# Kernel optimization log

Hardware: AMD Instinct MI355X
Metric: run time of the kernel (lower is better)

Reference implementation:

```python
import jax, jax.numpy as jnp
import numpy as np

B, C, H, W = 4, 256, 64, 64
CH = C // 2  # inner channels of the non-local block


def _conv1x1(x, w, b):
    # 1x1 conv == channel-mixing einsum; x: [B,C,H,W], w: [O,C], b: [O]
    return jnp.einsum('oc,bchw->bohw', w, x) + b[None, :, None, None]


def setup_inputs() -> dict:
    key = jax.random.key(0)
    ks = jax.random.split(key, 9)
    s = 0.02  # small init so exp(scores) stays in fp32 range (no max-subtraction in this block)
    return {
        'x':  jax.random.normal(ks[0], (B, C, H, W), dtype=jnp.float32),
        'w1': s * jax.random.normal(ks[1], (CH, C), dtype=jnp.float32),
        'b1': jnp.zeros((CH,), jnp.float32),
        'w2': s * jax.random.normal(ks[2], (CH, C), dtype=jnp.float32),
        'b2': jnp.zeros((CH,), jnp.float32),
        'w3': s * jax.random.normal(ks[3], (CH, C), dtype=jnp.float32),
        'b3': jnp.zeros((CH,), jnp.float32),
        'w4': s * jax.random.normal(ks[4], (C, CH), dtype=jnp.float32),
        'b4': jnp.zeros((C,), jnp.float32),
    }


def reference(x, w1, b1, w2, b2, w3, b3, w4, b4):
    b, c, h, w = x.shape
    n = h * w
    theta = _conv1x1(x, w1, b1).reshape(b, -1, n)  # [B, C/2, N]
    phi   = _conv1x1(x, w2, b2).reshape(b, -1, n)  # [B, C/2, N]
    g     = _conv1x1(x, w3, b3).reshape(b, -1, n)  # [B, C/2, N]
    # full non-local affinity: [B, N, N]
    scores = jnp.einsum('bci,bcj->bij', theta, phi)
    attn = jnp.exp(scores)  # faithful: no max-subtraction in the original
    attn = attn / jnp.sum(attn, axis=1, keepdims=True)  # normalize over dim=1 as written
    y = jnp.einsum('bij,bcj->bci', attn, g)  # [B, C/2, N]
    y = y.reshape(b, -1, h, w)               # [B, C/2, H, W]
    out = _conv1x1(y, w4, b4) + x            # project back to C, residual
    return out
```

## Files before the change

### kernel.cpp

```cpp
#include <hip/hip_runtime.h>

#define DEVI __device__ __forceinline__

typedef __attribute__((ext_vector_type(8))) short bf16x8;
typedef __attribute__((ext_vector_type(4))) short bf16x4;
typedef __attribute__((ext_vector_type(4))) float f32x4;

#define MFMA16 __builtin_amdgcn_mfma_f32_16x16x32_bf16

#define ASM_WAIT_VM_LGKM(n) asm volatile("s_waitcnt vmcnt(" #n ") lgkmcnt(0)" ::: "memory")
#define ASM_WAIT_LGKM() asm volatile("s_waitcnt lgkmcnt(0)" ::: "memory")
#define ASM_BARRIER() do { __builtin_amdgcn_s_barrier(); asm volatile("" ::: "memory"); } while (0)

DEVI short f2bs(float f) {
  union { float f; unsigned u; } v; v.f = f;
  unsigned r = v.u + 0x7fffu + ((v.u >> 16) & 1u);
  return (short)(r >> 16);
}
DEVI float bs2f(short s) {
  union { unsigned u; float f; } v; v.u = ((unsigned)(unsigned short)s) << 16;
  return v.f;
}

DEVI void gload_lds16(const short* g, short* lds) {
  __builtin_amdgcn_global_load_lds(
      (const __attribute__((address_space(1))) unsigned int*)g,
      (__attribute__((address_space(3))) unsigned int*)lds, 16, 0, 0);
}


DEVI void stage_chunk(short* lds, const short* g, int ldg, int tid) {
#pragma unroll
  for (int it = 0; it < 2; ++it) {
    int slot = it * 256 + tid;
    int row  = slot >> 2;
    int ko   = ((slot ^ (slot >> 3)) & 3) << 3;
    gload_lds16(g + (size_t)row * ldg + ko, lds + slot * 8);
  }
}

DEVI void stage_chunk64(short* lds, const short* g, int ldg, int tid) {
  int row = tid >> 2;
  int ko  = ((tid ^ (tid >> 3)) & 3) << 3;
  gload_lds16(g + (size_t)row * ldg + ko, lds + tid * 8);
}

DEVI bf16x8 lds8(const short* p) { return *(const bf16x8*)p; }

DEVI void zero_acc(f32x4 (&a)[4][4]) {
  f32x4 z = {0.f, 0.f, 0.f, 0.f};
#pragma unroll
  for (int i = 0; i < 4; ++i)
#pragma unroll
    for (int j = 0; j < 4; ++j) a[i][j] = z;
}

__global__ __launch_bounds__(256) void k_transpose_cast(const float* __restrict__ x,
                                                        short* __restrict__ xt) {
  __shared__ float t[64][65];
  int b = blockIdx.z;
  int c0 = blockIdx.y * 64;
  int p0 = blockIdx.x * 64;
  int tid = threadIdx.x;
  const float* xb = x + (size_t)b * 256 * 4096;
#pragma unroll
  for (int i = 0; i < 16; ++i) {
    int idx = i * 256 + tid;
    int c = idx >> 6, p = idx & 63;
    t[p][c] = xb[(size_t)(c0 + c) * 4096 + p0 + p];
  }
  __syncthreads();
  short* xtb = xt + ((size_t)b * 4096 + p0) * 256 + c0;
#pragma unroll
  for (int i = 0; i < 16; ++i) {
    int idx = i * 256 + tid;
    int p = idx >> 6, c = idx & 63;
    xtb[(size_t)p * 256 + c] = f2bs(t[p][c]);
  }
}

__global__ __launch_bounds__(256) void k_cast_w(const float* __restrict__ w1,
                                                const float* __restrict__ w2,
                                                const float* __restrict__ w3,
                                                short* __restrict__ w123) {
  int i = blockIdx.x * 256 + threadIdx.x;
  if (i < 384 * 256) {
    int r = i >> 8;
    const float* w = (r < 128) ? w1 : (r < 256 ? w2 : w3);
    w123[i] = f2bs(w[(size_t)(r & 127) * 256 + (i & 255)]);
  }
}

__global__ __launch_bounds__(256) void k_proj(const short* __restrict__ xt,
                                              const short* __restrict__ w123,
                                              const float* __restrict__ b1,
                                              const float* __restrict__ b2,
                                              const float* __restrict__ b3,
                                              short* __restrict__ theta,
                                              short* __restrict__ phi,
                                              short* __restrict__ gbuf) {
  __shared__ short aL[2][4096];
  __shared__ short bL[2][4096];
  __shared__ short oL[128 * 136];
  int tid = threadIdx.x;
  int m0 = blockIdx.x * 128;
  int nb = blockIdx.y;
  int b  = blockIdx.z;
  int lane = tid & 63, wid = tid >> 6;
  int col = lane & 15, quad = lane >> 4;
  int sl = (col >> 1) & 3;
  int qs = (quad ^ sl) << 3;
  int wm = (wid >> 1) * 64, wn = (wid & 1) * 64;
  const short* A = xt + ((size_t)b * 4096 + m0) * 256;
  const short* B = w123 + (size_t)nb * 128 * 256;
  f32x4 acc[4][4];
  zero_acc(acc);
  stage_chunk(&aL[0][0], A, 256, tid);
  stage_chunk(&bL[0][0], B, 256, tid);
  for (int ks = 0; ks < 8; ++ks) {
    int cur = ks & 1;
    ASM_WAIT_VM_LGKM(0);
    ASM_BARRIER();
    if (ks < 7) {
      stage_chunk(&aL[cur ^ 1][0], A + (ks + 1) * 32, 256, tid);
      stage_chunk(&bL[cur ^ 1][0], B + (ks + 1) * 32, 256, tid);
    }
    bf16x8 af[4], bf_[4];
#pragma unroll
    for (int mi = 0; mi < 4; ++mi) af[mi] = lds8(&aL[cur][(wm + mi * 16 + col) * 32 + qs]);
#pragma unroll
    for (int ni = 0; ni < 4; ++ni) bf_[ni] = lds8(&bL[cur][(wn + ni * 16 + col) * 32 + qs]);
    __builtin_amdgcn_s_setprio(1);
#pragma unroll
    for (int mi = 0; mi < 4; ++mi)
#pragma unroll
      for (int ni = 0; ni < 4; ++ni)
        acc[mi][ni] = MFMA16(af[mi], bf_[ni], acc[mi][ni], 0, 0, 0);
    __builtin_amdgcn_s_setprio(0);
  }
  const float* bias = (nb == 0) ? b1 : (nb == 1 ? b2 : b3);
#pragma unroll
  for (int mi = 0; mi < 4; ++mi)
#pragma unroll
    for (int ni = 0; ni < 4; ++ni) {
      float bv = bias[wn + ni * 16 + col];
#pragma unroll
      for (int r = 0; r < 4; ++r)
        oL[(wm + mi * 16 + quad * 4 + r) * 136 + wn + ni * 16 + col] = f2bs(acc[mi][ni][r] + bv);
    }
  __syncthreads();
  short* O = ((nb == 0) ? theta : (nb == 1) ? phi : gbuf) + ((size_t)b * 4096 + m0) * 128;
#pragma unroll
  for (int it = 0; it < 8; ++it) {
    int slot = it * 256 + tid;
    int r = slot >> 4, cp = (slot & 15) * 8;
    *(bf16x8*)(O + (size_t)r * 128 + cp) = lds8(&oL[r * 136 + cp]);
  }
}

__global__ __launch_bounds__(256, 2) void k_denom(const short* __restrict__ theta,
                                                  const short* __restrict__ phi,
                                                  float* __restrict__ dpart) {
  __shared__ short phB[2][16384];
  __shared__ float part[1024];
  int tid = threadIdx.x;
  int ib = blockIdx.x, jc = blockIdx.y, b = blockIdx.z;
  int lane = tid & 63, wid = tid >> 6;
  int col = lane & 15, quad = lane >> 4;
  int sl = (col >> 1) & 3;
  int qs = (quad ^ sl) << 3;
  int wm = (wid >> 1) * 64, wn = (wid & 1) * 64;
  const short* T = theta + ((size_t)b * 4096 + ib * 128) * 128;
  const short* P = phi + ((size_t)b * 4096 + (size_t)jc * 1024) * 128;
  float* dbase = dpart + ((size_t)(b * 32 + ib)) * 4096 + jc * 1024;
  short* Lb = &phB[0][0];
#pragma unroll
  for (int ks = 0; ks < 4; ++ks) stage_chunk(Lb + ks * 8192, T + ks * 32, 128, tid);
  __syncthreads();
  bf16x8 ath[4][4];
#pragma unroll
  for (int ks = 0; ks < 4; ++ks)
#pragma unroll
    for (int mi = 0; mi < 4; ++mi)
      ath[ks][mi] = lds8(&Lb[ks * 8192 + (wm + mi * 16 + col) * 32 + qs]);
  __syncthreads();
#pragma unroll
  for (int ks = 0; ks < 4; ++ks) stage_chunk(&phB[0][0] + ks * 4096, P + ks * 32, 128, tid);
  float dval = 0.f;
  for (int jt = 0; jt < 8; ++jt) {
    int cur = jt & 1;
    ASM_WAIT_VM_LGKM(0);
    ASM_BARRIER();
    if (jt > 0 && tid < 128) dbase[(jt - 1) * 128 + tid] = dval;
    if (jt < 7) {
      const short* Pn = P + (size_t)(jt + 1) * 128 * 128;
#pragma unroll
      for (int ks = 0; ks < 4; ++ks) stage_chunk(&phB[cur ^ 1][0] + ks * 4096, Pn + ks * 32, 128, tid);
    }
    f32x4 sacc[4][4];
    zero_acc(sacc);
#pragma unroll
    for (int ks = 0; ks < 4; ++ks) {
      bf16x8 bp[4];
#pragma unroll
      for (int ni = 0; ni < 4; ++ni) bp[ni] = lds8(&phB[cur][ks * 4096 + (wn + ni * 16 + col) * 32 + qs]);
      __builtin_amdgcn_s_setprio(1);
#pragma unroll
      for (int mi = 0; mi < 4; ++mi)
#pragma unroll
        for (int ni = 0; ni < 4; ++ni)
          sacc[mi][ni] = MFMA16(ath[ks][mi], bp[ni], sacc[mi][ni], 0, 0, 0);
      __builtin_amdgcn_s_setprio(0);
    }
#pragma unroll
    for (int ni = 0; ni < 4; ++ni) {
      float s = 0.f;
#pragma unroll
      for (int mi = 0; mi < 4; ++mi)
#pragma unroll
        for (int r = 0; r < 4; ++r) s += __expf(sacc[mi][ni][r]);
      part[((wid >> 1) * 4 + quad) * 128 + wn + ni * 16 + col] = s;
    }
    ASM_WAIT_LGKM();
    ASM_BARRIER();
    if (tid < 128) {
      float d = 0.f;
#pragma unroll
      for (int q = 0; q < 8; ++q) d += part[q * 128 + tid];
      dval = d;
    }
  }
  if (tid < 128) dbase[7 * 128 + tid] = dval;
}

__global__ __launch_bounds__(256) void k_fold(const short* __restrict__ gbuf,
                                              const float* __restrict__ dpart,
                                              short* __restrict__ gprime) {
  __shared__ float dinv[128];
  __shared__ short t[128 * 136];
  int tid = threadIdx.x;
  int jb = blockIdx.x, b = blockIdx.y;
  int j0 = jb * 128;
  if (tid < 128) {
    float d = 0.f;
    for (int ib = 0; ib < 32; ++ib) d += dpart[((size_t)(b * 32 + ib)) * 4096 + j0 + tid];
    dinv[tid] = 1.0f / d;
  }
  __syncthreads();
  const short* G = gbuf + ((size_t)b * 4096 + j0) * 128;
#pragma unroll
  for (int it = 0; it < 8; ++it) {
    int slot = it * 256 + tid;
    int j = slot >> 4, c8 = (slot & 15) * 8;
    bf16x8 gv = *(const bf16x8*)(G + (size_t)j * 128 + c8);
    float di = dinv[j];
#pragma unroll
    for (int e = 0; e < 8; ++e) t[(c8 + e) * 136 + j] = f2bs(bs2f(gv[e]) * di);
  }
  __syncthreads();
  short* GP = gprime + (size_t)b * 128 * 4096 + j0;
#pragma unroll
  for (int it = 0; it < 8; ++it) {
    int slot = it * 256 + tid;
    int c = slot >> 4, j8 = (slot & 15) * 8;
    *(bf16x8*)(GP + (size_t)c * 4096 + j8) = *(const bf16x8*)&t[c * 136 + j8];
  }
}

__global__ __launch_bounds__(256, 2) void k_attn_pv(const short* __restrict__ theta,
                                                    const short* __restrict__ phi,
                                                    const short* __restrict__ gprime,
                                                    short* __restrict__ ypart) {
  __shared__ short L[40960];
  int tid = threadIdx.x;
  int ib = blockIdx.x, jc = blockIdx.y, b = blockIdx.z;
  int lane = tid & 63, wid = tid >> 6;
  int col = lane & 15, quad = lane >> 4;
  int sl = (col >> 1) & 3;
  int qs = (quad ^ sl) << 3;
  int wm = (wid >> 1) * 64;
  int cj = wid & 1;
  int wnS = cj * 32;
  int wnV = cj * 64;
  const short* T = theta + ((size_t)b * 4096 + ib * 128) * 128;
  const short* PH = phi + ((size_t)b * 4096 + (size_t)jc * 1024) * 128;
  const short* GP = gprime + (size_t)b * 128 * 4096 + jc * 1024;
  short* pP = L + 32768;
#pragma unroll
  for (int ks = 0; ks < 4; ++ks) stage_chunk(L + ks * 8192, T + ks * 32, 128, tid);
  __syncthreads();
  bf16x8 ath[4][4];
#pragma unroll
  for (int ks = 0; ks < 4; ++ks)
#pragma unroll
    for (int mi = 0; mi < 4; ++mi)
      ath[ks][mi] = lds8(&L[ks * 8192 + (wm + mi * 16 + col) * 32 + qs]);
  __syncthreads();
#pragma unroll
  for (int ks = 0; ks < 4; ++ks) stage_chunk64(L + ks * 2048, PH + ks * 32, 128, tid);
#pragma unroll
  for (int jh = 0; jh < 2; ++jh) stage_chunk(L + 16384 + jh * 4096, GP + jh * 32, 4096, tid);
  f32x4 accy[4][4];
  zero_acc(accy);
  int qh = quad >> 1, ql = (quad & 1) << 2;
  for (int jt = 0; jt < 16; ++jt) {
    int cur = jt & 1;
    short* phc = L + cur * 8192;
    short* phn = L + (cur ^ 1) * 8192;
    short* gpc = L + 16384 + cur * 8192;
    short* gpn = L + 16384 + (cur ^ 1) * 8192;
    ASM_WAIT_VM_LGKM(4);
    ASM_BARRIER();
    if (jt < 15) {
      const short* PHn = PH + (size_t)(jt + 1) * 64 * 128;
#pragma unroll
      for (int ks = 0; ks < 4; ++ks) stage_chunk64(phn + ks * 2048, PHn + ks * 32, 128, tid);
    }
    f32x4 st[2][4];
#pragma unroll
    for (int mj = 0; mj < 2; ++mj)
#pragma unroll
      for (int ni = 0; ni < 4; ++ni) st[mj][ni] = (f32x4){0.f, 0.f, 0.f, 0.f};
#pragma unroll
    for (int ks = 0; ks < 4; ++ks) {
      bf16x8 bp[2];
#pragma unroll
      for (int mj = 0; mj < 2; ++mj)
        bp[mj] = lds8(&phc[ks * 2048 + (wnS + mj * 16 + col) * 32 + qs]);
      __builtin_amdgcn_s_setprio(1);
#pragma unroll
      for (int mj = 0; mj < 2; ++mj)
#pragma unroll
        for (int ni = 0; ni < 4; ++ni)
          st[mj][ni] = MFMA16(bp[mj], ath[ks][ni], st[mj][ni], 0, 0, 0);
      __builtin_amdgcn_s_setprio(0);
    }
#pragma unroll
    for (int mj = 0; mj < 2; ++mj)
#pragma unroll
      for (int ni = 0; ni < 4; ++ni) {
        int i = wm + ni * 16 + col;
        bf16x4 p4;
#pragma unroll
        for (int r = 0; r < 4; ++r) p4[r] = f2bs(__expf(st[mj][ni][r]));
        *(bf16x4*)&pP[cj * 4096 + i * 32 + ((((mj << 1) + qh) ^ sl) << 3) + ql] = p4;
      }
    if (jt < 15) { ASM_WAIT_VM_LGKM(4); } else { ASM_WAIT_VM_LGKM(0); }
    ASM_BARRIER();
    if (jt < 15) {
      const short* GPn = GP + (jt + 1) * 64;
#pragma unroll
      for (int jh = 0; jh < 2; ++jh) stage_chunk(gpn + jh * 4096, GPn + jh * 32, 4096, tid);
    }
#pragma unroll
    for (int ks = 0; ks < 2; ++ks) {
      bf16x8 ap[4], bg[4];
#pragma unroll
      for (int mi = 0; mi < 4; ++mi)
        ap[mi] = lds8(&pP[ks * 4096 + (wm + mi * 16 + col) * 32 + qs]);
#pragma unroll
      for (int ni = 0; ni < 4; ++ni)
        bg[ni] = lds8(&gpc[ks * 4096 + (wnV + ni * 16 + col) * 32 + qs]);
      __builtin_amdgcn_s_setprio(1);
#pragma unroll
      for (int mi = 0; mi < 4; ++mi)
#pragma unroll
        for (int ni = 0; ni < 4; ++ni)
          accy[mi][ni] = MFMA16(ap[mi], bg[ni], accy[mi][ni], 0, 0, 0);
      __builtin_amdgcn_s_setprio(0);
    }
  }
  short* Yp = ypart + ((size_t)(jc * 4 + b) * 4096 + (size_t)ib * 128) * 128;
#pragma unroll
  for (int half = 0; half < 2; ++half) {
    __syncthreads();
    if ((wid >> 1) == half) {
#pragma unroll
      for (int mi = 0; mi < 4; ++mi)
#pragma unroll
        for (int ni = 0; ni < 4; ++ni)
#pragma unroll
          for (int r = 0; r < 4; ++r)
            pP[(mi * 16 + quad * 4 + r) * 128 + wnV + ni * 16 + col] = f2bs(accy[mi][ni][r]);
    }
    __syncthreads();
#pragma unroll
    for (int it = 0; it < 4; ++it) {
      int slot = it * 256 + tid;
      int r = slot >> 4, c8 = (slot & 15) * 8;
      *(bf16x8*)(Yp + (size_t)(half * 64 + r) * 128 + c8) = lds8(&pP[r * 128 + c8]);
    }
  }
}

__global__ __launch_bounds__(256) void k_out(const short* __restrict__ ypart,
                                             const float* __restrict__ w4,
                                             const float* __restrict__ b4,
                                             const float* __restrict__ x,
                                             float* __restrict__ out) {
  __shared__ short wL[4 * 4096];
  __shared__ short yL[4 * 4096];
  __shared__ float bLs[128];
  int tid = threadIdx.x;
  int ibk = blockIdx.x, ob = blockIdx.y, b = blockIdx.z;
  int o0 = ob * 128, i0 = ibk * 128;
  int lane = tid & 63, wid = tid >> 6;
  int col = lane & 15, quad = lane >> 4;
  int sl = (col >> 1) & 3;
  int qsw = (quad ^ sl) << 3;
  int wm = (wid >> 1) * 64, wn = (wid & 1) * 64;
#pragma unroll
  for (int it = 0; it < 16; ++it) {
    int slot = it * 256 + tid;
    int r = slot >> 5, c4 = (slot & 31) * 4;
    int ks = c4 >> 5, cr = c4 & 31;
    f32x4 wv = *(const f32x4*)(w4 + (size_t)(o0 + r) * 128 + c4);
    bf16x4 wp;
#pragma unroll
    for (int e = 0; e < 4; ++e) wp[e] = f2bs(wv[e]);
    *(bf16x4*)&wL[ks * 4096 + r * 32 + ((((cr >> 3) ^ ((r >> 1) & 3)) << 3) | (cr & 4))] = wp;
  }
#pragma unroll
  for (int it = 0; it < 8; ++it) {
    int slot = it * 256 + tid;
    int r = slot >> 4, c8 = (slot & 15) * 8;
    int ks = c8 >> 5, cr = c8 & 31;
    float a8[8];
#pragma unroll
    for (int e = 0; e < 8; ++e) a8[e] = 0.f;
#pragma unroll
    for (int p = 0; p < 4; ++p) {
      bf16x8 v = *(const bf16x8*)(ypart + ((size_t)(p * 4 + b) * 4096 + i0 + r) * 128 + c8);
#pragma unroll
      for (int e = 0; e < 8; ++e) a8[e] += bs2f(v[e]);
    }
    bf16x8 yv;
#pragma unroll
    for (int e = 0; e < 8; ++e) yv[e] = f2bs(a8[e]);
    *(bf16x8*)&yL[ks * 4096 + r * 32 + (((cr >> 3) ^ ((r >> 1) & 3)) << 3)] = yv;
  }
  if (tid < 128) bLs[tid] = b4[o0 + tid];
  __syncthreads();
  f32x4 acc[4][4];
  zero_acc(acc);
#pragma unroll
  for (int ks = 0; ks < 4; ++ks) {
    bf16x8 af[4], bf_[4];
#pragma unroll
    for (int mi = 0; mi < 4; ++mi) af[mi] = lds8(&wL[ks * 4096 + (wm + mi * 16 + col) * 32 + qsw]);
#pragma unroll
    for (int ni = 0; ni < 4; ++ni) bf_[ni] = lds8(&yL[ks * 4096 + (wn + ni * 16 + col) * 32 + qsw]);
#pragma unroll
    for (int mi = 0; mi < 4; ++mi)
#pragma unroll
      for (int ni = 0; ni < 4; ++ni)
        acc[mi][ni] = MFMA16(af[mi], bf_[ni], acc[mi][ni], 0, 0, 0);
  }
  const float* X = x + ((size_t)b * 256 + o0) * 4096 + i0;
  float* O = out + ((size_t)b * 256 + o0) * 4096 + i0;
#pragma unroll
  for (int mi = 0; mi < 4; ++mi)
#pragma unroll
    for (int ni = 0; ni < 4; ++ni)
#pragma unroll
      for (int r = 0; r < 4; ++r) {
        int o = wm + mi * 16 + quad * 4 + r;
        int i = wn + ni * 16 + col;
        O[(size_t)o * 4096 + i] = acc[mi][ni][r] + X[(size_t)o * 4096 + i] + bLs[o];
      }
}

extern "C" void kernel_launch(void* const* d_in, const int* in_sizes, int n_in,
                              void* d_out, int out_size, void* d_ws, size_t ws_size,
                              hipStream_t stream) {
  const float* x  = (const float*)d_in[0];
  const float* w1 = (const float*)d_in[1];
  const float* b1 = (const float*)d_in[2];
  const float* w2 = (const float*)d_in[3];
  const float* b2 = (const float*)d_in[4];
  const float* w3 = (const float*)d_in[5];
  const float* b3 = (const float*)d_in[6];
  const float* w4 = (const float*)d_in[7];
  const float* b4 = (const float*)d_in[8];
  char* ws = (char*)d_ws;
  short* xt     = (short*)(ws + 0);
  short* w123   = (short*)(ws + 8388608);
  short* theta  = (short*)(ws + 8585216);
  short* phi    = (short*)(ws + 12779520);
  short* gbuf   = (short*)(ws + 16973824);
  short* gprime = (short*)(ws + 21168128);
  float* dpart  = (float*)(ws + 25362432);
  short* ypart  = (short*)(ws + 27459584);
  float* out    = (float*)d_out;
  (void)in_sizes; (void)n_in; (void)out_size; (void)ws_size;

  k_transpose_cast<<<dim3(64, 4, 4), dim3(256), 0, stream>>>(x, xt);
  k_cast_w<<<dim3(384), dim3(256), 0, stream>>>(w1, w2, w3, w123);
  k_proj<<<dim3(32, 3, 4), dim3(256), 0, stream>>>(xt, w123, b1, b2, b3, theta, phi, gbuf);
  k_denom<<<dim3(32, 4, 4), dim3(256), 0, stream>>>(theta, phi, dpart);
  k_fold<<<dim3(32, 4), dim3(256), 0, stream>>>(gbuf, dpart, gprime);
  k_attn_pv<<<dim3(32, 4, 4), dim3(256), 0, stream>>>(theta, phi, gprime, ypart);
  k_out<<<dim3(32, 2, 4), dim3(256), 0, stream>>>(ypart, w4, b4, x, out);
}
```

Baseline: 169.0 us.

## Split attention-PV block across eight waves with 512 threads per block

Doubles k_attn_pv's block size from 256 to 512 threads. Each wave now owns 32 query rows instead of 64, so per-wave accumulators and theta fragments are halved, and staging helpers are rewritten so 512 threads cooperatively load theta, phi and g'. The fine-grained vmcnt waits with raw barriers are replaced by plain __syncthreads, and launch bounds request 4 waves per SIMD. The aim is more waves to hide latency with lower register pressure, at the cost of full-drain synchronisation, which loses the partial overlap of outstanding loads.

After: 172.9 us. 2.3% more time.

```diff
diff --git a/kernel.cpp b/kernel.cpp
--- a/kernel.cpp
+++ b/kernel.cpp
@@ -39,10 +39,38 @@
   }
 }
 
-DEVI void stage_chunk64(short* lds, const short* g, int ldg, int tid) {
-  int row = tid >> 2;
-  int ko  = ((tid ^ (tid >> 3)) & 3) << 3;
-  gload_lds16(g + (size_t)row * ldg + ko, lds + tid * 8);
+DEVI void stage_theta512(short* lds, const short* g, int tid) {
+#pragma unroll
+  for (int it = 0; it < 4; ++it) {
+    int slot = it * 512 + tid;
+    int ck = slot >> 9;
+    int s  = slot & 511;
+    int row = s >> 2;
+    int ko  = ((s ^ (s >> 3)) & 3) << 3;
+    gload_lds16(g + ck * 32 + (size_t)row * 128 + ko, lds + ck * 8192 + s * 8);
+  }
+}
+DEVI void stage_phi512(short* lds, const short* g, int tid) {
+#pragma unroll
+  for (int it = 0; it < 2; ++it) {
+    int slot = it * 512 + tid;
+    int ck = slot >> 8;
+    int s  = slot & 255;
+    int row = s >> 2;
+    int ko  = ((s ^ (s >> 3)) & 3) << 3;
+    gload_lds16(g + ck * 32 + (size_t)row * 128 + ko, lds + ck * 2048 + s * 8);
+  }
+}
+DEVI void stage_gp512(short* lds, const short* g, int tid) {
+#pragma unroll
+  for (int it = 0; it < 2; ++it) {
+    int slot = it * 512 + tid;
+    int ck = slot >> 9;
+    int s  = slot & 511;
+    int row = s >> 2;
+    int ko  = ((s ^ (s >> 3)) & 3) << 3;
+    gload_lds16(g + ck * 32 + (size_t)row * 4096 + ko, lds + ck * 4096 + s * 8);
+  }
 }
 
 DEVI bf16x8 lds8(const short* p) { return *(const bf16x8*)p; }
@@ -267,7 +295,7 @@
   }
 }
 
-__global__ __launch_bounds__(256, 2) void k_attn_pv(const short* __restrict__ theta,
+__global__ __launch_bounds__(512, 4) void k_attn_pv(const short* __restrict__ theta,
                                                     const short* __restrict__ phi,
                                                     const short* __restrict__ gprime,
                                                     short* __restrict__ ypart) {
@@ -278,30 +306,34 @@
   int col = lane & 15, quad = lane >> 4;
   int sl = (col >> 1) & 3;
   int qs = (quad ^ sl) << 3;
-  int wm = (wid >> 1) * 64;
-  int cj = wid & 1;
-  int wnS = cj * 32;
-  int wnV = cj * 64;
+  int iq = wid >> 1;
+  int jh = wid & 1;
+  int wmI = iq * 32;
+  int wjS = jh * 32;
+  int wcV = jh * 64;
   const short* T = theta + ((size_t)b * 4096 + ib * 128) * 128;
   const short* PH = phi + ((size_t)b * 4096 + (size_t)jc * 1024) * 128;
   const short* GP = gprime + (size_t)b * 128 * 4096 + jc * 1024;
   short* pP = L + 32768;
-#pragma unroll
-  for (int ks = 0; ks < 4; ++ks) stage_chunk(L + ks * 8192, T + ks * 32, 128, tid);
-  __syncthreads();
-  bf16x8 ath[4][4];
+  stage_theta512(L, T, tid);
+  __syncthreads();
+  bf16x8 ath[4][2];
 #pragma unroll
   for (int ks = 0; ks < 4; ++ks)
 #pragma unroll
-    for (int mi = 0; mi < 4; ++mi)
-      ath[ks][mi] = lds8(&L[ks * 8192 + (wm + mi * 16 + col) * 32 + qs]);
-  __syncthreads();
-#pragma unroll
-  for (int ks = 0; ks < 4; ++ks) stage_chunk64(L + ks * 2048, PH + ks * 32, 128, tid);
-#pragma unroll
-  for (int jh = 0; jh < 2; ++jh) stage_chunk(L + 16384 + jh * 4096, GP + jh * 32, 4096, tid);
-  f32x4 accy[4][4];
-  zero_acc(accy);
+    for (int mi = 0; mi < 2; ++mi)
+      ath[ks][mi] = lds8(&L[ks * 8192 + (wmI + mi * 16 + col) * 32 + qs]);
+  __syncthreads();
+  stage_phi512(L, PH, tid);
+  stage_gp512(L + 16384, GP, tid);
+  f32x4 accy[2][4];
+  {
+    f32x4 z = {0.f, 0.f, 0.f, 0.f};
+#pragma unroll
+    for (int i = 0; i < 2; ++i)
+#pragma unroll
+      for (int j = 0; j < 4; ++j) accy[i][j] = z;
+  }
   int qh = quad >> 1, ql = (quad & 1) << 2;
   for (int jt = 0; jt < 16; ++jt) {
     int cur = jt & 1;
@@ -309,61 +341,55 @@
     short* phn = L + (cur ^ 1) * 8192;
     short* gpc = L + 16384 + cur * 8192;
     short* gpn = L + 16384 + (cur ^ 1) * 8192;
-    ASM_WAIT_VM_LGKM(4);
-    ASM_BARRIER();
+    __syncthreads();
     if (jt < 15) {
-      const short* PHn = PH + (size_t)(jt + 1) * 64 * 128;
-#pragma unroll
-      for (int ks = 0; ks < 4; ++ks) stage_chunk64(phn + ks * 2048, PHn + ks * 32, 128, tid);
-    }
-    f32x4 st[2][4];
+      stage_phi512(phn, PH + (size_t)(jt + 1) * 64 * 128, tid);
+    }
+    f32x4 st[2][2];
 #pragma unroll
     for (int mj = 0; mj < 2; ++mj)
 #pragma unroll
-      for (int ni = 0; ni < 4; ++ni) st[mj][ni] = (f32x4){0.f, 0.f, 0.f, 0.f};
+      for (int ni = 0; ni < 2; ++ni) st[mj][ni] = (f32x4){0.f, 0.f, 0.f, 0.f};
 #pragma unroll
     for (int ks = 0; ks < 4; ++ks) {
       bf16x8 bp[2];
 #pragma unroll
       for (int mj = 0; mj < 2; ++mj)
-        bp[mj] = lds8(&phc[ks * 2048 + (wnS + mj * 16 + col) * 32 + qs]);
+        bp[mj] = lds8(&phc[ks * 2048 + (wjS + mj * 16 + col) * 32 + qs]);
       __builtin_amdgcn_s_setprio(1);
 #pragma unroll
       for (int mj = 0; mj < 2; ++mj)
 #pragma unroll
-        for (int ni = 0; ni < 4; ++ni)
+        for (int ni = 0; ni < 2; ++ni)
           st[mj][ni] = MFMA16(bp[mj], ath[ks][ni], st[mj][ni], 0, 0, 0);
       __builtin_amdgcn_s_setprio(0);
     }
 #pragma unroll
     for (int mj = 0; mj < 2; ++mj)
 #pragma unroll
-      for (int ni = 0; ni < 4; ++ni) {
-        int i = wm + ni * 16 + col;
+      for (int ni = 0; ni < 2; ++ni) {
+        int i = wmI + ni * 16 + col;
         bf16x4 p4;
 #pragma unroll
         for (int r = 0; r < 4; ++r) p4[r] = f2bs(__expf(st[mj][ni][r]));
-        *(bf16x4*)&pP[cj * 4096 + i * 32 + ((((mj << 1) + qh) ^ sl) << 3) + ql] = p4;
+        *(bf16x4*)&pP[jh * 4096 + i * 32 + ((((mj << 1) + qh) ^ sl) << 3) + ql] = p4;
       }
-    if (jt < 15) { ASM_WAIT_VM_LGKM(4); } else { ASM_WAIT_VM_LGKM(0); }
-    ASM_BARRIER();
+    __syncthreads();
     if (jt < 15) {
-      const short* GPn = GP + (jt + 1) * 64;
-#pragma unroll
-      for (int jh = 0; jh < 2; ++jh) stage_chunk(gpn + jh * 4096, GPn + jh * 32, 4096, tid);
+      stage_gp512(gpn, GP + (jt + 1) * 64, tid);
     }
 #pragma unroll
     for (int ks = 0; ks < 2; ++ks) {
-      bf16x8 ap[4], bg[4];
-#pragma unroll
-      for (int mi = 0; mi < 4; ++mi)
-        ap[mi] = lds8(&pP[ks * 4096 + (wm + mi * 16 + col) * 32 + qs]);
+      bf16x8 ap[2], bg[4];
+#pragma unroll
+      for (int mi = 0; mi < 2; ++mi)
+        ap[mi] = lds8(&pP[ks * 4096 + (wmI + mi * 16 + col) * 32 + qs]);
 #pragma unroll
       for (int ni = 0; ni < 4; ++ni)
-        bg[ni] = lds8(&gpc[ks * 4096 + (wnV + ni * 16 + col) * 32 + qs]);
+        bg[ni] = lds8(&gpc[ks * 4096 + (wcV + ni * 16 + col) * 32 + qs]);
       __builtin_amdgcn_s_setprio(1);
 #pragma unroll
-      for (int mi = 0; mi < 4; ++mi)
+      for (int mi = 0; mi < 2; ++mi)
 #pragma unroll
         for (int ni = 0; ni < 4; ++ni)
           accy[mi][ni] = MFMA16(ap[mi], bg[ni], accy[mi][ni], 0, 0, 0);
@@ -374,19 +400,20 @@
 #pragma unroll
   for (int half = 0; half < 2; ++half) {
     __syncthreads();
-    if ((wid >> 1) == half) {
-#pragma unroll
-      for (int mi = 0; mi < 4; ++mi)
+    if ((iq >> 1) == half) {
+#pragma unroll
+      for (int mi = 0; mi < 2; ++mi)
 #pragma unroll
         for (int ni = 0; ni < 4; ++ni)
 #pragma unroll
           for (int r = 0; r < 4; ++r)
-            pP[(mi * 16 + quad * 4 + r) * 128 + wnV + ni * 16 + col] = f2bs(accy[mi][ni][r]);
+            pP[((iq & 1) * 32 + mi * 16 + quad * 4 + r) * 128 + wcV + ni * 16 + col] =
+                f2bs(accy[mi][ni][r]);
     }
     __syncthreads();
 #pragma unroll
-    for (int it = 0; it < 4; ++it) {
-      int slot = it * 256 + tid;
+    for (int it = 0; it < 2; ++it) {
+      int slot = it * 512 + tid;
       int r = slot >> 4, c8 = (slot & 15) * 8;
       *(bf16x8*)(Yp + (size_t)(half * 64 + r) * 128 + c8) = lds8(&pP[r * 128 + c8]);
     }
@@ -499,6 +526,6 @@
   k_proj<<<dim3(32, 3, 4), dim3(256), 0, stream>>>(xt, w123, b1, b2, b3, theta, phi, gbuf);
   k_denom<<<dim3(32, 4, 4), dim3(256), 0, stream>>>(theta, phi, dpart);
   k_fold<<<dim3(32, 4), dim3(256), 0, stream>>>(gbuf, dpart, gprime);
-  k_attn_pv<<<dim3(32, 4, 4), dim3(256), 0, stream>>>(theta, phi, gprime, ypart);
+  k_attn_pv<<<dim3(32, 4, 4), dim3(512), 0, stream>>>(theta, phi, gprime, ypart);
   k_out<<<dim3(32, 2, 4), dim3(256), 0, stream>>>(ypart, w4, b4, x, out);
 }
```

## Shrink k_denom tiles to 128x64 with 4 blocks/CU and simplify attn_pv waits

Applied to the files above, without the earlier changes.

k_denom now processes 64-column phi tiles over 512-column chunks per block, doubling the grid to 512 blocks, halving LDS and accumulator registers, and raising launch bounds to 4 blocks per CU. The aim is higher occupancy and better latency hiding for the exp-sum denominator pass. Separately, the hand-written vmcnt waits plus barriers in k_attn_pv are replaced by plain __syncthreads, which waits for all outstanding loads and may reduce prefetch overlap there.

After: 170.7 us. No clear change (+1.0%).

```diff
diff --git a/kernel.cpp b/kernel.cpp
--- a/kernel.cpp
+++ b/kernel.cpp
@@ -158,79 +158,85 @@
   }
 }
 
-__global__ __launch_bounds__(256, 2) void k_denom(const short* __restrict__ theta,
+__global__ __launch_bounds__(256, 4) void k_denom(const short* __restrict__ theta,
                                                   const short* __restrict__ phi,
                                                   float* __restrict__ dpart) {
-  __shared__ short phB[2][16384];
-  __shared__ float part[1024];
+  __shared__ short phB[2][8192];
+  __shared__ float part[16 * 64];
   int tid = threadIdx.x;
-  int ib = blockIdx.x, jc = blockIdx.y, b = blockIdx.z;
+  int ib = blockIdx.x, jq = blockIdx.y, b = blockIdx.z;
   int lane = tid & 63, wid = tid >> 6;
   int col = lane & 15, quad = lane >> 4;
   int sl = (col >> 1) & 3;
   int qs = (quad ^ sl) << 3;
-  int wm = (wid >> 1) * 64, wn = (wid & 1) * 64;
+  int wm = wid * 32;
   const short* T = theta + ((size_t)b * 4096 + ib * 128) * 128;
-  const short* P = phi + ((size_t)b * 4096 + (size_t)jc * 1024) * 128;
-  float* dbase = dpart + ((size_t)(b * 32 + ib)) * 4096 + jc * 1024;
+  const short* P = phi + ((size_t)b * 4096 + (size_t)jq * 512) * 128;
+  float* dbase = dpart + ((size_t)(b * 32 + ib)) * 4096 + jq * 512;
   short* Lb = &phB[0][0];
 #pragma unroll
-  for (int ks = 0; ks < 4; ++ks) stage_chunk(Lb + ks * 8192, T + ks * 32, 128, tid);
-  __syncthreads();
-  bf16x8 ath[4][4];
+  for (int ks = 0; ks < 4; ++ks) stage_chunk(Lb + ks * 4096, T + ks * 32, 128, tid);
+  __syncthreads();
+  bf16x8 ath[4][2];
 #pragma unroll
   for (int ks = 0; ks < 4; ++ks)
 #pragma unroll
-    for (int mi = 0; mi < 4; ++mi)
-      ath[ks][mi] = lds8(&Lb[ks * 8192 + (wm + mi * 16 + col) * 32 + qs]);
-  __syncthreads();
-#pragma unroll
-  for (int ks = 0; ks < 4; ++ks) stage_chunk(&phB[0][0] + ks * 4096, P + ks * 32, 128, tid);
+    for (int mi = 0; mi < 2; ++mi)
+      ath[ks][mi] = lds8(&Lb[ks * 4096 + (wm + mi * 16 + col) * 32 + qs]);
+  __syncthreads();
+#pragma unroll
+  for (int ks = 0; ks < 4; ++ks) stage_chunk64(&phB[0][0] + ks * 2048, P + ks * 32, 128, tid);
   float dval = 0.f;
   for (int jt = 0; jt < 8; ++jt) {
     int cur = jt & 1;
     ASM_WAIT_VM_LGKM(0);
     ASM_BARRIER();
-    if (jt > 0 && tid < 128) dbase[(jt - 1) * 128 + tid] = dval;
+    if (jt > 0 && tid < 64) dbase[(jt - 1) * 64 + tid] = dval;
     if (jt < 7) {
-      const short* Pn = P + (size_t)(jt + 1) * 128 * 128;
-#pragma unroll
-      for (int ks = 0; ks < 4; ++ks) stage_chunk(&phB[cur ^ 1][0] + ks * 4096, Pn + ks * 32, 128, tid);
-    }
-    f32x4 sacc[4][4];
-    zero_acc(sacc);
+      const short* Pn = P + (size_t)(jt + 1) * 64 * 128;
+#pragma unroll
+      for (int ks = 0; ks < 4; ++ks) stage_chunk64(&phB[cur ^ 1][0] + ks * 2048, Pn + ks * 32, 128, tid);
+    }
+    f32x4 sacc[2][4];
+    {
+      f32x4 z = {0.f, 0.f, 0.f, 0.f};
+#pragma unroll
+      for (int mi = 0; mi < 2; ++mi)
+#pragma unroll
+        for (int nj = 0; nj < 4; ++nj) sacc[mi][nj] = z;
+    }
 #pragma unroll
     for (int ks = 0; ks < 4; ++ks) {
       bf16x8 bp[4];
 #pragma unroll
-      for (int ni = 0; ni < 4; ++ni) bp[ni] = lds8(&phB[cur][ks * 4096 + (wn + ni * 16 + col) * 32 + qs]);
+      for (int nj = 0; nj < 4; ++nj) bp[nj] = lds8(&phB[cur][ks * 2048 + (nj * 16 + col) * 32 + qs]);
       __builtin_amdgcn_s_setprio(1);
 #pragma unroll
-      for (int mi = 0; mi < 4; ++mi)
-#pragma unroll
-        for (int ni = 0; ni < 4; ++ni)
-          sacc[mi][ni] = MFMA16(ath[ks][mi], bp[ni], sacc[mi][ni], 0, 0, 0);
+      for (int mi = 0; mi < 2; ++mi)
+#pragma unroll
+        for (int nj = 0; nj < 4; ++nj)
+          sacc[mi][nj] = MFMA16(ath[ks][mi], bp[nj], sacc[mi][nj], 0, 0, 0);
       __builtin_amdgcn_s_setprio(0);
     }
 #pragma unroll
-    for (int ni = 0; ni < 4; ++ni) {
+    for (int nj = 0; nj < 4; ++nj) {
       float s = 0.f;
 #pragma unroll
-      for (int mi = 0; mi < 4; ++mi)
-#pragma unroll
-        for (int r = 0; r < 4; ++r) s += __expf(sacc[mi][ni][r]);
-      part[((wid >> 1) * 4 + quad) * 128 + wn + ni * 16 + col] = s;
+      for (int mi = 0; mi < 2; ++mi)
+#pragma unroll
+        for (int r = 0; r < 4; ++r) s += __expf(sacc[mi][nj][r]);
+      part[(wid * 4 + quad) * 64 + nj * 16 + col] = s;
     }
     ASM_WAIT_LGKM();
     ASM_BARRIER();
-    if (tid < 128) {
+    if (tid < 64) {
       float d = 0.f;
 #pragma unroll
-      for (int q = 0; q < 8; ++q) d += part[q * 128 + tid];
+      for (int g = 0; g < 16; ++g) d += part[g * 64 + tid];
       dval = d;
     }
   }
-  if (tid < 128) dbase[7 * 128 + tid] = dval;
+  if (tid < 64) dbase[7 * 64 + tid] = dval;
 }
 
 __global__ __launch_bounds__(256) void k_fold(const short* __restrict__ gbuf,
@@ -309,8 +315,7 @@
     short* phn = L + (cur ^ 1) * 8192;
     short* gpc = L + 16384 + cur * 8192;
     short* gpn = L + 16384 + (cur ^ 1) * 8192;
-    ASM_WAIT_VM_LGKM(4);
-    ASM_BARRIER();
+    __syncthreads();
     if (jt < 15) {
       const short* PHn = PH + (size_t)(jt + 1) * 64 * 128;
 #pragma unroll
@@ -345,8 +350,7 @@
         for (int r = 0; r < 4; ++r) p4[r] = f2bs(__expf(st[mj][ni][r]));
         *(bf16x4*)&pP[cj * 4096 + i * 32 + ((((mj << 1) + qh) ^ sl) << 3) + ql] = p4;
       }
-    if (jt < 15) { ASM_WAIT_VM_LGKM(4); } else { ASM_WAIT_VM_LGKM(0); }
-    ASM_BARRIER();
+    __syncthreads();
     if (jt < 15) {
       const short* GPn = GP + (jt + 1) * 64;
 #pragma unroll
@@ -497,7 +501,7 @@
   k_transpose_cast<<<dim3(64, 4, 4), dim3(256), 0, stream>>>(x, xt);
   k_cast_w<<<dim3(384), dim3(256), 0, stream>>>(w1, w2, w3, w123);
   k_proj<<<dim3(32, 3, 4), dim3(256), 0, stream>>>(xt, w123, b1, b2, b3, theta, phi, gbuf);
-  k_denom<<<dim3(32, 4, 4), dim3(256), 0, stream>>>(theta, phi, dpart);
+  k_denom<<<dim3(32, 8, 4), dim3(256), 0, stream>>>(theta, phi, dpart);
   k_fold<<<dim3(32, 4), dim3(256), 0, stream>>>(gbuf, dpart, gprime);
   k_attn_pv<<<dim3(32, 4, 4), dim3(256), 0, stream>>>(theta, phi, gprime, ypart);
   k_out<<<dim3(32, 2, 4), dim3(256), 0, stream>>>(ypart, w4, b4, x, out);
```

## Split attention key range eight ways with smaller tiles for higher occupancy

Applied to the files above, without the earlier changes.

The attention kernel now splits the key dimension into 8 chunks instead of 4, processes 32 keys per iteration instead of 64, and halves shared memory so four blocks can fit per CU. k_out now sums 8 partial outputs. This adds grid parallelism and occupancy at the cost of twice the partial-output traffic, more barriers per key, and uses plain __syncthreads instead of the finer vmcnt waits. The ypart workspace must hold 8 partials, and its capacity is not visible.

Result: slower. 327.0 us (+93.5%).

```diff
diff --git a/kernel.cpp b/kernel.cpp
--- a/kernel.cpp
+++ b/kernel.cpp
@@ -43,6 +43,18 @@
   int row = tid >> 2;
   int ko  = ((tid ^ (tid >> 3)) & 3) << 3;
   gload_lds16(g + (size_t)row * ldg + ko, lds + tid * 8);
+}
+
+DEVI void stage_phi32(short* lds, const short* g, int tid) {
+#pragma unroll
+  for (int it = 0; it < 2; ++it) {
+    int slot = it * 256 + tid;
+    int ck = slot >> 7;
+    int s  = slot & 127;
+    int row = s >> 2;
+    int ko  = ((s ^ (s >> 3)) & 3) << 3;
+    gload_lds16(g + ck * 32 + (size_t)row * 128 + ko, lds + ck * 1024 + s * 8);
+  }
 }
 
 DEVI bf16x8 lds8(const short* p) { return *(const bf16x8*)p; }
@@ -267,11 +279,11 @@
   }
 }
 
-__global__ __launch_bounds__(256, 2) void k_attn_pv(const short* __restrict__ theta,
+__global__ __launch_bounds__(256, 4) void k_attn_pv(const short* __restrict__ theta,
                                                     const short* __restrict__ phi,
                                                     const short* __restrict__ gprime,
                                                     short* __restrict__ ypart) {
-  __shared__ short L[40960];
+  __shared__ short L[20480];
   int tid = threadIdx.x;
   int ib = blockIdx.x, jc = blockIdx.y, b = blockIdx.z;
   int lane = tid & 63, wid = tid >> 6;
@@ -280,96 +292,76 @@
   int qs = (quad ^ sl) << 3;
   int wm = (wid >> 1) * 64;
   int cj = wid & 1;
-  int wnS = cj * 32;
   int wnV = cj * 64;
   const short* T = theta + ((size_t)b * 4096 + ib * 128) * 128;
-  const short* PH = phi + ((size_t)b * 4096 + (size_t)jc * 1024) * 128;
-  const short* GP = gprime + (size_t)b * 128 * 4096 + jc * 1024;
-  short* pP = L + 32768;
-#pragma unroll
-  for (int ks = 0; ks < 4; ++ks) stage_chunk(L + ks * 8192, T + ks * 32, 128, tid);
+  const short* PH = phi + ((size_t)b * 4096 + (size_t)jc * 512) * 128;
+  const short* GP = gprime + (size_t)b * 128 * 4096 + jc * 512;
+  short* pP = L + 16384;
+#pragma unroll
+  for (int ks = 0; ks < 4; ++ks) stage_chunk(L + ks * 4096, T + ks * 32, 128, tid);
   __syncthreads();
   bf16x8 ath[4][4];
 #pragma unroll
   for (int ks = 0; ks < 4; ++ks)
 #pragma unroll
     for (int mi = 0; mi < 4; ++mi)
-      ath[ks][mi] = lds8(&L[ks * 8192 + (wm + mi * 16 + col) * 32 + qs]);
-  __syncthreads();
-#pragma unroll
-  for (int ks = 0; ks < 4; ++ks) stage_chunk64(L + ks * 2048, PH + ks * 32, 128, tid);
-#pragma unroll
-  for (int jh = 0; jh < 2; ++jh) stage_chunk(L + 16384 + jh * 4096, GP + jh * 32, 4096, tid);
+      ath[ks][mi] = lds8(&L[ks * 4096 + (wm + mi * 16 + col) * 32 + qs]);
+  __syncthreads();
+  stage_phi32(L, PH, tid);
+  stage_chunk(L + 8192, GP, 4096, tid);
   f32x4 accy[4][4];
   zero_acc(accy);
   int qh = quad >> 1, ql = (quad & 1) << 2;
   for (int jt = 0; jt < 16; ++jt) {
     int cur = jt & 1;
-    short* phc = L + cur * 8192;
-    short* phn = L + (cur ^ 1) * 8192;
-    short* gpc = L + 16384 + cur * 8192;
-    short* gpn = L + 16384 + (cur ^ 1) * 8192;
-    ASM_WAIT_VM_LGKM(4);
-    ASM_BARRIER();
+    short* phc = L + cur * 4096;
+    short* phn = L + (cur ^ 1) * 4096;
+    short* gpc = L + 8192 + cur * 4096;
+    short* gpn = L + 8192 + (cur ^ 1) * 4096;
+    __syncthreads();
     if (jt < 15) {
-      const short* PHn = PH + (size_t)(jt + 1) * 64 * 128;
-#pragma unroll
-      for (int ks = 0; ks < 4; ++ks) stage_chunk64(phn + ks * 2048, PHn + ks * 32, 128, tid);
-    }
-    f32x4 st[2][4];
-#pragma unroll
-    for (int mj = 0; mj < 2; ++mj)
-#pragma unroll
-      for (int ni = 0; ni < 4; ++ni) st[mj][ni] = (f32x4){0.f, 0.f, 0.f, 0.f};
+      stage_phi32(phn, PH + (size_t)(jt + 1) * 32 * 128, tid);
+    }
+    f32x4 st[4];
+#pragma unroll
+    for (int ni = 0; ni < 4; ++ni) st[ni] = (f32x4){0.f, 0.f, 0.f, 0.f};
 #pragma unroll
     for (int ks = 0; ks < 4; ++ks) {
-      bf16x8 bp[2];
-#pragma unroll
-      for (int mj = 0; mj < 2; ++mj)
-        bp[mj] = lds8(&phc[ks * 2048 + (wnS + mj * 16 + col) * 32 + qs]);
+      bf16x8 bp = lds8(&phc[ks * 1024 + (cj * 16 + col) * 32 + qs]);
       __builtin_amdgcn_s_setprio(1);
 #pragma unroll
-      for (int mj = 0; mj < 2; ++mj)
-#pragma unroll
-        for (int ni = 0; ni < 4; ++ni)
-          st[mj][ni] = MFMA16(bp[mj], ath[ks][ni], st[mj][ni], 0, 0, 0);
+      for (int ni = 0; ni < 4; ++ni)
+        st[ni] = MFMA16(bp, ath[ks][ni], st[ni], 0, 0, 0);
       __builtin_amdgcn_s_setprio(0);
     }
 #pragma unroll
-    for (int mj = 0; mj < 2; ++mj)
-#pragma unroll
-      for (int ni = 0; ni < 4; ++ni) {
-        int i = wm + ni * 16 + col;
-        bf16x4 p4;
-#pragma unroll
-        for (int r = 0; r < 4; ++r) p4[r] = f2bs(__expf(st[mj][ni][r]));
-        *(bf16x4*)&pP[cj * 4096 + i * 32 + ((((mj << 1) + qh) ^ sl) << 3) + ql] = p4;
-      }
-    if (jt < 15) { ASM_WAIT_VM_LGKM(4); } else { ASM_WAIT_VM_LGKM(0); }
-    ASM_BARRIER();
+    for (int ni = 0; ni < 4; ++ni) {
+      int i = wm + ni * 16 + col;
+      bf16x4 p4;
+#pragma unroll
+      for (int r = 0; r < 4; ++r) p4[r] = f2bs(__expf(st[ni][r]));
+      *(bf16x4*)&pP[i * 32 + (((cj * 2 + qh) ^ sl) << 3) + ql] = p4;
+    }
+    __syncthreads();
     if (jt < 15) {
-      const short* GPn = GP + (jt + 1) * 64;
-#pragma unroll
-      for (int jh = 0; jh < 2; ++jh) stage_chunk(gpn + jh * 4096, GPn + jh * 32, 4096, tid);
-    }
-#pragma unroll
-    for (int ks = 0; ks < 2; ++ks) {
-      bf16x8 ap[4], bg[4];
-#pragma unroll
-      for (int mi = 0; mi < 4; ++mi)
-        ap[mi] = lds8(&pP[ks * 4096 + (wm + mi * 16 + col) * 32 + qs]);
+      stage_chunk(gpn, GP + (jt + 1) * 32, 4096, tid);
+    }
+    bf16x8 ap[4], bg[4];
+#pragma unroll
+    for (int mi = 0; mi < 4; ++mi)
+      ap[mi] = lds8(&pP[(wm + mi * 16 + col) * 32 + qs]);
+#pragma unroll
+    for (int ni = 0; ni < 4; ++ni)
+      bg[ni] = lds8(&gpc[(wnV + ni * 16 + col) * 32 + qs]);
+    __builtin_amdgcn_s_setprio(1);
+#pragma unroll
+    for (int mi = 0; mi < 4; ++mi)
 #pragma unroll
       for (int ni = 0; ni < 4; ++ni)
-        bg[ni] = lds8(&gpc[ks * 4096 + (wnV + ni * 16 + col) * 32 + qs]);
-      __builtin_amdgcn_s_setprio(1);
-#pragma unroll
-      for (int mi = 0; mi < 4; ++mi)
-#pragma unroll
-        for (int ni = 0; ni < 4; ++ni)
-          accy[mi][ni] = MFMA16(ap[mi], bg[ni], accy[mi][ni], 0, 0, 0);
-      __builtin_amdgcn_s_setprio(0);
-    }
-  }
+        accy[mi][ni] = MFMA16(ap[mi], bg[ni], accy[mi][ni], 0, 0, 0);
+    __builtin_amdgcn_s_setprio(0);
+  }
+  short* eb = L;
   short* Yp = ypart + ((size_t)(jc * 4 + b) * 4096 + (size_t)ib * 128) * 128;
 #pragma unroll
   for (int half = 0; half < 2; ++half) {
@@ -381,14 +373,14 @@
         for (int ni = 0; ni < 4; ++ni)
 #pragma unroll
           for (int r = 0; r < 4; ++r)
-            pP[(mi * 16 + quad * 4 + r) * 128 + wnV + ni * 16 + col] = f2bs(accy[mi][ni][r]);
+            eb[(mi * 16 + quad * 4 + r) * 128 + wnV + ni * 16 + col] = f2bs(accy[mi][ni][r]);
     }
     __syncthreads();
 #pragma unroll
     for (int it = 0; it < 4; ++it) {
       int slot = it * 256 + tid;
       int r = slot >> 4, c8 = (slot & 15) * 8;
-      *(bf16x8*)(Yp + (size_t)(half * 64 + r) * 128 + c8) = lds8(&pP[r * 128 + c8]);
+      *(bf16x8*)(Yp + (size_t)(half * 64 + r) * 128 + c8) = lds8(&eb[r * 128 + c8]);
     }
   }
 }
@@ -429,7 +421,7 @@
 #pragma unroll
     for (int e = 0; e < 8; ++e) a8[e] = 0.f;
 #pragma unroll
-    for (int p = 0; p < 4; ++p) {
+    for (int p = 0; p < 8; ++p) {
       bf16x8 v = *(const bf16x8*)(ypart + ((size_t)(p * 4 + b) * 4096 + i0 + r) * 128 + c8);
 #pragma unroll
       for (int e = 0; e < 8; ++e) a8[e] += bs2f(v[e]);
@@ -499,6 +491,6 @@
   k_proj<<<dim3(32, 3, 4), dim3(256), 0, stream>>>(xt, w123, b1, b2, b3, theta, phi, gbuf);
   k_denom<<<dim3(32, 4, 4), dim3(256), 0, stream>>>(theta, phi, dpart);
   k_fold<<<dim3(32, 4), dim3(256), 0, stream>>>(gbuf, dpart, gprime);
-  k_attn_pv<<<dim3(32, 4, 4), dim3(256), 0, stream>>>(theta, phi, gprime, ypart);
+  k_attn_pv<<<dim3(32, 8, 4), dim3(256), 0, stream>>>(theta, phi, gprime, ypart);
   k_out<<<dim3(32, 2, 4), dim3(256), 0, stream>>>(ypart, w4, b4, x, out);
 }
```
